# Performance work log

Hardware: AMD Instinct MI355X
Metric: run time of the kernel (lower is better)

The kernel has to match this reference:

```python
import jax, jax.numpy as jnp
import numpy as np
import math

B, N, E, H, DEPTH, MLP_RATIO, A = 8, 1024, 768, 12, 6, 4, 7
F = MLP_RATIO * E


def _get_attention_slopes(n):
    def p2(n):
        start = 2 ** (-2 ** (-(math.log2(n) - 3)))
        return [start * start ** i for i in range(n)]
    if math.log2(n).is_integer():
        return p2(n)
    c = 2 ** math.floor(math.log2(n))
    return p2(c) + _get_attention_slopes(2 * c)[0::2][: n - c]


def _ln(x, scale, bias, eps=1e-6):
    m = jnp.mean(x, axis=-1, keepdims=True)
    v = jnp.var(x, axis=-1, keepdims=True)
    return (x - m) * jax.lax.rsqrt(v + eps) * scale + bias


def setup_inputs() -> dict:
    key = jax.random.key(0)
    ks = jax.random.split(key, 8)
    s = 0.02
    return {
        "x": jax.random.normal(ks[0], (B, N, E), jnp.float32),
        "ln1_scale": jnp.ones((DEPTH, E), jnp.float32),
        "ln1_bias": jnp.zeros((DEPTH, E), jnp.float32),
        "wqkv": jax.random.normal(ks[1], (DEPTH, E, 3 * E), jnp.float32) * s,
        "bqkv": jnp.zeros((DEPTH, 3 * E), jnp.float32),
        "wo": jax.random.normal(ks[2], (DEPTH, E, E), jnp.float32) * s,
        "bo": jnp.zeros((DEPTH, E), jnp.float32),
        "ln2_scale": jnp.ones((DEPTH, E), jnp.float32),
        "ln2_bias": jnp.zeros((DEPTH, E), jnp.float32),
        "w1": jax.random.normal(ks[3], (DEPTH, E, F), jnp.float32) * s,
        "w2": jax.random.normal(ks[4], (DEPTH, F, E), jnp.float32) * s,
        "lnf_scale": jnp.ones((E,), jnp.float32),
        "lnf_bias": jnp.zeros((E,), jnp.float32),
        "head_w1": jax.random.normal(ks[5], (E, E), jnp.float32) * s,
        "head_b1": jnp.zeros((E,), jnp.float32),
        "head_w2": jax.random.normal(ks[6], (E, A), jnp.float32) * s,
    }


def reference(x, ln1_scale, ln1_bias, wqkv, bqkv, wo, bo, ln2_scale, ln2_bias, w1, w2, lnf_scale, lnf_bias, head_w1, head_b1, head_w2):
    b, n, e = x.shape
    h = H
    dh = e // h
    scale = dh ** (-0.5)
    # ALiBi bias: slopes[h] * key-position (exactly as original code computes it)
    slopes = jnp.asarray(_get_attention_slopes(h), x.dtype)
    pos_bias = slopes[None, :, None, None] * jnp.arange(n, dtype=x.dtype)[None, None, None, :]
    causal = jnp.tril(jnp.ones((n, n), bool))[None, None]  # [1,1,n,n]
    big_neg = jnp.finfo(x.dtype).min

    depth = ln1_scale.shape[0]
    for i in range(depth):
        y = _ln(x, ln1_scale[i], ln1_bias[i])
        qkv = y @ wqkv[i] + bqkv[i]
        q, k, v = jnp.split(qkv, 3, axis=-1)
        q = q.reshape(b, n, h, dh).transpose(0, 2, 1, 3)  # b h n d
        k = k.reshape(b, n, h, dh).transpose(0, 2, 1, 3)
        v = v.reshape(b, n, h, dh).transpose(0, 2, 1, 3)
        att = jnp.einsum('bhnd,bhmd->bhnm', q, k) * scale + pos_bias
        att = jnp.where(causal, att, big_neg)
        att = jax.nn.softmax(att, axis=-1)
        o = jnp.einsum('bhnm,bhmd->bhnd', att, v)
        o = o.transpose(0, 2, 1, 3).reshape(b, n, e)
        x = x + (o @ wo[i] + bo[i])
        y = _ln(x, ln2_scale[i], ln2_bias[i])
        y = jax.nn.gelu(y @ w1[i])  # flax default: tanh-approx gelu; FF has no bias
        x = x + y @ w2[i]
    x = _ln(x, lnf_scale, lnf_bias)
    actions = jax.nn.relu(x @ head_w1 + head_b1) @ head_w2
    return actions
```

## Files before the change

### kernel.cpp

```cpp
#include <hip/hip_runtime.h>
#include <hip/hip_bf16.h>
#include <cstdint>

#define DEV __device__ __forceinline__

typedef __bf16 bf16x8 __attribute__((ext_vector_type(8)));
typedef float f32x4 __attribute__((ext_vector_type(4)));
typedef unsigned short u16;
typedef u16 u16x8 __attribute__((ext_vector_type(8)));
typedef u16 u16x4 __attribute__((ext_vector_type(4)));
typedef uint32_t u32x2 __attribute__((ext_vector_type(2)));
typedef uint32_t u32x4 __attribute__((ext_vector_type(4)));

DEV u16 f2bf(float f) {
  union { float f; uint32_t u; } a; a.f = f;
  uint32_t u = a.u + 0x7fffu + ((a.u >> 16) & 1u);
  return (u16)(u >> 16);
}
DEV float b2f(u16 v) {
  union { uint32_t u; float f; } a; a.u = ((uint32_t)v) << 16;
  return a.f;
}

DEV float fexp2(float x) {
#if __has_builtin(__builtin_amdgcn_exp2f)
  return __builtin_amdgcn_exp2f(x);
#else
  return __expf(x * 0.69314718056f);
#endif
}

DEV uint32_t cvtpk(float lo, float hi) {
  uint32_t r;
  asm("v_cvt_pk_bf16_f32 %0, %1, %2" : "=v"(r) : "v"(lo), "v"(hi));
  return r;
}

DEV void gload16(const void* g, void* lds) {
  __builtin_amdgcn_global_load_lds((__attribute__((address_space(1))) void*)g,
                                   (__attribute__((address_space(3))) void*)lds,
                                   16, 0, 0);
}

struct TMat { const float* src; u16* dst; int K; int N; int t0; };
struct TArgs { TMat m[26]; int nmat; };

__global__ __launch_bounds__(256) void transpose_all(TArgs args) {
  __shared__ float tile[128][65];
  const int bid = blockIdx.x;
  int i = 0;
  #pragma unroll 1
  for (int t = 1; t < args.nmat; ++t) if (bid >= args.m[t].t0) i = t;
  const TMat mm = args.m[i];
  const int tid = threadIdx.x;
  const int tix = bid - mm.t0;
  const int ntx = mm.N >> 6;
  const int n0 = (tix % ntx) << 6, k0 = (tix / ntx) << 7;
  const int lr = tid >> 4, lc4 = (tid & 15) << 2;
  #pragma unroll
  for (int p = 0; p < 8; ++p) {
    const int r = lr + (p << 4);
    f32x4 v = __builtin_nontemporal_load(
        (const f32x4*)(mm.src + (size_t)(k0 + r) * mm.N + n0 + lc4));
    *(f32x4*)&tile[r][lc4] = v;
  }
  __syncthreads();
  const int ks8 = (tid & 15) << 3;
  #pragma unroll
  for (int p = 0; p < 4; ++p) {
    const int n = (tid >> 4) + (p << 4);
    float v[8];
    #pragma unroll
    for (int u = 0; u < 8; ++u) v[u] = tile[ks8 + u][n];
    u32x4 o;
    o[0] = cvtpk(v[0], v[1]); o[1] = cvtpk(v[2], v[3]);
    o[2] = cvtpk(v[4], v[5]); o[3] = cvtpk(v[6], v[7]);
    __builtin_nontemporal_store(
        o, (u32x4*)(mm.dst + (size_t)(n0 + n) * mm.K + k0 + ks8));
  }
}

__global__ __launch_bounds__(256) void f2b_kernel(const f32x4* __restrict__ in,
                                                  u32x4* __restrict__ out, int n8) {
  const int i = blockIdx.x * 256 + threadIdx.x;
  if (i >= n8) return;
  f32x4 a = __builtin_nontemporal_load(in + 2 * i);
  f32x4 b = __builtin_nontemporal_load(in + 2 * i + 1);
  u32x4 o;
  o[0] = cvtpk(a[0], a[1]); o[1] = cvtpk(a[2], a[3]);
  o[2] = cvtpk(b[0], b[1]); o[3] = cvtpk(b[2], b[3]);
  __builtin_nontemporal_store(o, out + i);
}

__global__ __launch_bounds__(256) void ln_kernel(const u16* __restrict__ x,
                                                 const float* __restrict__ sc,
                                                 const float* __restrict__ bi,
                                                 u16* __restrict__ y, int Mtok) {
  const int bid = blockIdx.x;
  const int tok = ((bid & 7) << 10) + ((bid >> 3) << 2) + (threadIdx.x >> 6);
  const int l = threadIdx.x & 63;
  if (tok >= Mtok) return;
  const u16* row = x + (size_t)tok * 768;
  u16x8 v0 = *(const u16x8*)(row + l * 8);
  u16x4 v1 = *(const u16x4*)(row + 512 + l * 4);
  float f[12];
  #pragma unroll
  for (int i = 0; i < 8; ++i) f[i] = b2f(v0[i]);
  #pragma unroll
  for (int i = 0; i < 4; ++i) f[8 + i] = b2f(v1[i]);
  float s = 0.f, q = 0.f;
  #pragma unroll
  for (int i = 0; i < 12; ++i) { s += f[i]; q += f[i] * f[i]; }
  #pragma unroll
  for (int off = 1; off < 64; off <<= 1) { s += __shfl_xor(s, off); q += __shfl_xor(q, off); }
  const float mean = s * (1.f / 768.f);
  const float var = q * (1.f / 768.f) - mean * mean;
  const float r = rsqrtf(var + 1e-6f);
  float4 s0 = *(const float4*)(sc + l * 8);
  float4 s1 = *(const float4*)(sc + l * 8 + 4);
  float4 s2 = *(const float4*)(sc + 512 + l * 4);
  float4 b0 = *(const float4*)(bi + l * 8);
  float4 b1 = *(const float4*)(bi + l * 8 + 4);
  float4 b2 = *(const float4*)(bi + 512 + l * 4);
  float g[12];
  g[0] = (f[0]-mean)*r*s0.x + b0.x;  g[1] = (f[1]-mean)*r*s0.y + b0.y;
  g[2] = (f[2]-mean)*r*s0.z + b0.z;  g[3] = (f[3]-mean)*r*s0.w + b0.w;
  g[4] = (f[4]-mean)*r*s1.x + b1.x;  g[5] = (f[5]-mean)*r*s1.y + b1.y;
  g[6] = (f[6]-mean)*r*s1.z + b1.z;  g[7] = (f[7]-mean)*r*s1.w + b1.w;
  g[8] = (f[8]-mean)*r*s2.x + b2.x;  g[9] = (f[9]-mean)*r*s2.y + b2.y;
  g[10] = (f[10]-mean)*r*s2.z + b2.z; g[11] = (f[11]-mean)*r*s2.w + b2.w;
  u16* yr = y + (size_t)tok * 768;
  u32x4 o;
  o[0] = cvtpk(g[0], g[1]); o[1] = cvtpk(g[2], g[3]);
  o[2] = cvtpk(g[4], g[5]); o[3] = cvtpk(g[6], g[7]);
  *(u32x4*)(yr + l * 8) = o;
  u32x2 o2; o2[0] = cvtpk(g[8], g[9]); o2[1] = cvtpk(g[10], g[11]);
  *(u32x2*)(yr + 512 + l * 4) = o2;
}

enum { EPI_BF16 = 0, EPI_RESID = 1, EPI_GELU = 2, EPI_RELU = 3 };

__global__ __launch_bounds__(1024, 2) void gemm128(
    const u16* __restrict__ A, const u16* __restrict__ Bt,
    const float* __restrict__ bias, const u16* __restrict__ residB,
    u16* __restrict__ outB, int N, int K, int nxb, int epi) {
  __shared__ u16 smem[32768];
  const int tid = threadIdx.x;
  const int w = tid >> 6, l = tid & 63;

  const int nwg = gridDim.x;
  const int flat = blockIdx.x;
  const int wg = (flat & 7) * (nwg >> 3) + (flat >> 3);
  const int bx = wg % nxb, by = wg / nxb;
  const int m0 = by << 7, n0 = bx << 7;

  const int wr = (w >> 2) << 5;
  const int wc = (w & 3) << 5;
  const int cl = l & 15, g = l >> 4;
  f32x4 acc[2][2] = {};

  const int lrow = l >> 3;
  const int scol = ((l & 7) ^ lrow) << 3;
  const u16* agp = A  + (size_t)(m0 + (w << 3) + lrow) * K + scol;
  const u16* bgp = Bt + (size_t)(n0 + (w << 3) + lrow) * K + scol;
  const int ldso = w << 9;
  const int nkt = K >> 6;

  gload16(agp, &smem[ldso]);
  gload16(bgp, &smem[16384 + ldso]);

  const int sw = cl & 7;
  for (int kt = 0; kt < nkt; ++kt) {
    const int cur = kt & 1;
    if (kt + 1 < nkt) {
      const size_t koff = (size_t)(kt + 1) << 6;
      const int nb = (cur ^ 1) << 13;
      gload16(agp + koff, &smem[nb + ldso]);
      gload16(bgp + koff, &smem[16384 + nb + ldso]);
      asm volatile("s_waitcnt vmcnt(2)" ::: "memory");
    } else {
      asm volatile("s_waitcnt vmcnt(0)" ::: "memory");
    }
    __builtin_amdgcn_s_barrier();
    __builtin_amdgcn_sched_barrier(0);
    const u16* Ab = &smem[cur << 13];
    const u16* Bb = &smem[16384 + (cur << 13)];
    #pragma unroll
    for (int ks = 0; ks < 2; ++ks) {
      bf16x8 af[2], bfr[2];
      const int ps = (((ks << 2) | g) ^ sw) << 3;
      #pragma unroll
      for (int mt = 0; mt < 2; ++mt)
        af[mt] = *(const bf16x8*)(Ab + ((wr + mt * 16 + cl) << 6) + ps);
      #pragma unroll
      for (int nt = 0; nt < 2; ++nt)
        bfr[nt] = *(const bf16x8*)(Bb + ((wc + nt * 16 + cl) << 6) + ps);
      #pragma unroll
      for (int mt = 0; mt < 2; ++mt)
        #pragma unroll
        for (int nt = 0; nt < 2; ++nt)
          acc[mt][nt] = __builtin_amdgcn_mfma_f32_16x16x32_bf16(af[mt], bfr[nt], acc[mt][nt], 0, 0, 0);
    }
    asm volatile("s_waitcnt lgkmcnt(0)" ::: "memory");
    __builtin_amdgcn_s_barrier();
  }

  float* scr = (float*)smem + w * 544;
  const int rg = g << 2;
  const int er = l >> 2;
  const int ec0 = (l & 3) << 3;
  #pragma unroll
  for (int mt = 0; mt < 2; ++mt) {
    #pragma unroll
    for (int nt = 0; nt < 2; ++nt)
      #pragma unroll
      for (int j = 0; j < 4; ++j)
        scr[(rg + j) * 34 + nt * 16 + cl] = acc[mt][nt][j];
    const int grow = m0 + wr + mt * 16 + er;
    const int gcol = n0 + wc + ec0;
    float v[8];
    #pragma unroll
    for (int u = 0; u < 8; ++u) v[u] = scr[er * 34 + ec0 + u];
    if (bias) {
      #pragma unroll
      for (int u = 0; u < 8; ++u) v[u] += bias[gcol + u];
    }
    if (epi == EPI_RESID) {
      u16x8 rv = *(const u16x8*)(residB + (size_t)grow * N + gcol);
      #pragma unroll
      for (int u = 0; u < 8; ++u) v[u] += b2f(rv[u]);
    } else if (epi == EPI_GELU) {
      #pragma unroll
      for (int u = 0; u < 8; ++u) {
        const float x = v[u];
        const float e = __expf(-(1.5957691216f * x + 0.0713548163f * x * x * x));
        v[u] = x / (1.f + e);
      }
    } else if (epi == EPI_RELU) {
      #pragma unroll
      for (int u = 0; u < 8; ++u) v[u] = fmaxf(v[u], 0.f);
    }
    u32x4 ov;
    ov[0] = cvtpk(v[0], v[1]); ov[1] = cvtpk(v[2], v[3]);
    ov[2] = cvtpk(v[4], v[5]); ov[3] = cvtpk(v[6], v[7]);
    u32x4* op = (u32x4*)(outB + (size_t)grow * N + gcol);
    if (epi == EPI_BF16 || epi == EPI_GELU)
      __builtin_nontemporal_store(ov, op);
    else
      *op = ov;
  }
}

__global__ __launch_bounds__(512, 6) void attn_kernel(const u16* __restrict__ qkv,
                                                      u16* __restrict__ o) {
  __shared__ u16 Ksm[2][4096];
  __shared__ u16 Vt[2][64][68];
  __shared__ u16 P[8][16][72];
  const int flat = blockIdx.x;
  const int b = flat & 7;
  const int rr = flat >> 3;
  const int h = rr >> 3;
  const int j = rr & 7;
  const int tid = threadIdx.x;
  const int w = tid >> 6, l = tid & 63;
  const int cl = l & 15, lg = l >> 4;
  const int qtile = (w < 4) ? j : 15 - j;
  const int q0 = qtile * 64 + (w & 3) * 16;
  const int rowg = q0 + cl;
  const float log2e = 1.44269504f;
  const float scale2 = 0.125f * log2e;
  const float slope = (h < 8) ? exp2f(-(float)(h + 1)) : exp2f(-0.5f - (float)(h - 8));
  const float slope2 = slope * log2e;
  const size_t rs_ = 2304;
  const size_t bbase = (size_t)b * 1024 * rs_;

  const u16* qp = qkv + bbase + (size_t)rowg * rs_ + h * 64 + lg * 8;
  bf16x8 qa0 = *(const bf16x8*)qp;
  bf16x8 qa1 = *(const bf16x8*)(qp + 32);

  float m_r = -1e30f, l_r = 0.f;
  f32x4 oacc[4];
  #pragma unroll
  for (int d = 0; d < 4; ++d) oacc[d] = (f32x4){0.f, 0.f, 0.f, 0.f};

  const u16* ksrc = qkv + bbase + (size_t)(tid >> 3) * rs_ + 768 + h * 64 +
                    (((tid & 7) ^ ((tid >> 3) & 7)) << 3);
  const int vd0 = w << 3;
  const u16* vbase = qkv + bbase + (size_t)l * rs_ + 1536 + h * 64 + vd0;

  const int nkv = 16 - j;
  gload16(ksrc, &Ksm[0][w << 9]);
  u16x8 vreg = *(const u16x8*)vbase;
  __syncthreads();

  const int sw = cl & 7;
  const int ps0 = (lg ^ sw) << 3;
  const int ps1 = ps0 ^ 32;

  for (int kv = 0; kv < nkv; ++kv) {
    const int buf = kv & 1;
    #pragma unroll
    for (int i = 0; i < 8; ++i) Vt[buf][vd0 + i][l] = vreg[i];
    u16x8 vnext = vreg;
    if (kv + 1 < nkv) {
      gload16(ksrc + (size_t)(kv + 1) * 64 * rs_, &Ksm[buf ^ 1][w << 9]);
      vnext = *(const u16x8*)(vbase + (size_t)(kv + 1) * 64 * rs_);
    }

    const bool active = (kv <= qtile);
    bf16x8 pa0, pa1;
    if (active) {
      const u16* Kb = &Ksm[buf][0];
      f32x4 pp[4];
      float pm = -3.0e38f;
      __builtin_amdgcn_s_setprio(1);
      #pragma unroll
      for (int nt = 0; nt < 4; ++nt) {
        const int row = nt * 16 + cl;
        bf16x8 bk0 = *(const bf16x8*)(Kb + (row << 6) + ps0);
        bf16x8 bk1 = *(const bf16x8*)(Kb + (row << 6) + ps1);
        f32x4 s = (f32x4){0.f, 0.f, 0.f, 0.f};
        s = __builtin_amdgcn_mfma_f32_16x16x32_bf16(bk0, qa0, s, 0, 0, 0);
        s = __builtin_amdgcn_mfma_f32_16x16x32_bf16(bk1, qa1, s, 0, 0, 0);
        const int kb = kv * 64 + nt * 16 + (lg << 2);
        #pragma unroll
        for (int jj = 0; jj < 4; ++jj) {
          const int colg = kb + jj;
          float v = s[jj] * scale2 + slope2 * (float)colg;
          pp[nt][jj] = (colg <= rowg) ? v : -3.0e38f;
        }
        pm = fmaxf(pm, fmaxf(fmaxf(pp[nt][0], pp[nt][1]),
                             fmaxf(pp[nt][2], pp[nt][3])));
      }
      __builtin_amdgcn_s_setprio(0);
      pm = fmaxf(pm, __shfl_xor(pm, 16));
      pm = fmaxf(pm, __shfl_xor(pm, 32));
      if (!__all(pm <= m_r + 11.54f)) {
        const float mnew = fmaxf(m_r, pm);
        const float al = fexp2(m_r - mnew);
        m_r = mnew;
        l_r *= al;
        float a4[4];
        #pragma unroll
        for (int jj = 0; jj < 4; ++jj) a4[jj] = __shfl(al, (lg << 2) + jj);
        #pragma unroll
        for (int d = 0; d < 4; ++d)
          #pragma unroll
          for (int jj = 0; jj < 4; ++jj) oacc[d][jj] *= a4[jj];
      }
      float rs = 0.f;
      #pragma unroll
      for (int nt = 0; nt < 4; ++nt) {
        #pragma unroll
        for (int jj = 0; jj < 4; ++jj) {
          float p = fexp2(pp[nt][jj] - m_r);
          pp[nt][jj] = p;
          rs += p;
        }
      }
      rs += __shfl_xor(rs, 16);
      rs += __shfl_xor(rs, 32);
      l_r += rs;
      #pragma unroll
      for (int nt = 0; nt < 4; ++nt) {
        u32x2 pr;
        pr[0] = cvtpk(pp[nt][0], pp[nt][1]);
        pr[1] = cvtpk(pp[nt][2], pp[nt][3]);
        *(u32x2*)&P[w][cl][nt * 16 + (lg << 2)] = pr;
      }
      pa0 = *(const bf16x8*)&P[w][cl][lg * 8];
      pa1 = *(const bf16x8*)&P[w][cl][32 + lg * 8];
    }

    __syncthreads();

    if (active) {
      __builtin_amdgcn_s_setprio(1);
      #pragma unroll
      for (int d = 0; d < 4; ++d) {
        bf16x8 bv0 = *(const bf16x8*)&Vt[buf][d * 16 + cl][lg * 8];
        bf16x8 bv1 = *(const bf16x8*)&Vt[buf][d * 16 + cl][32 + lg * 8];
        oacc[d] = __builtin_amdgcn_mfma_f32_16x16x32_bf16(pa0, bv0, oacc[d], 0, 0, 0);
        oacc[d] = __builtin_amdgcn_mfma_f32_16x16x32_bf16(pa1, bv1, oacc[d], 0, 0, 0);
      }
      __builtin_amdgcn_s_setprio(0);
    }
    vreg = vnext;
  }

  const float linv = 1.f / l_r;
  float i4[4];
  #pragma unroll
  for (int jj = 0; jj < 4; ++jj) i4[jj] = __shfl(linv, (lg << 2) + jj);
  u16* op = o + ((size_t)b * 1024 + q0) * 768 + h * 64;
  #pragma unroll
  for (int d = 0; d < 4; ++d)
    #pragma unroll
    for (int jj = 0; jj < 4; ++jj)
      op[(size_t)((lg << 2) + jj) * 768 + d * 16 + cl] = f2bf(oacc[d][jj] * i4[jj]);
}

__global__ __launch_bounds__(256) void head2_kernel(const u16* __restrict__ act,
                                                    const float* __restrict__ w,
                                                    float* __restrict__ out, int Mtok) {
  const int bid = blockIdx.x;
  const int tok = ((bid & 7) << 10) + ((bid >> 3) << 2) + (threadIdx.x >> 6);
  const int l = threadIdx.x & 63;
  if (tok >= Mtok) return;
  float s[7] = {0.f, 0.f, 0.f, 0.f, 0.f, 0.f, 0.f};
  const u16* ar = act + (size_t)tok * 768;
  #pragma unroll
  for (int i = 0; i < 12; ++i) {
    const int k = l + i * 64;
    const float a = b2f(ar[k]);
    #pragma unroll
    for (int j = 0; j < 7; ++j) s[j] += a * w[k * 7 + j];
  }
  #pragma unroll
  for (int off = 32; off; off >>= 1)
    #pragma unroll
    for (int j = 0; j < 7; ++j) s[j] += __shfl_down(s[j], off);
  if (l == 0) {
    #pragma unroll
    for (int j = 0; j < 7; ++j) out[(size_t)tok * 7 + j] = s[j];
  }
}

extern "C" void kernel_launch(void* const* d_in, const int* in_sizes, int n_in,
                              void* d_out, int out_size, void* d_ws, size_t ws_size,
                              hipStream_t stream) {
  const float* x_in = (const float*)d_in[0];
  const float* ln1s = (const float*)d_in[1];
  const float* ln1b = (const float*)d_in[2];
  const float* wqkv = (const float*)d_in[3];
  const float* bqkv = (const float*)d_in[4];
  const float* wo   = (const float*)d_in[5];
  const float* bo   = (const float*)d_in[6];
  const float* ln2s = (const float*)d_in[7];
  const float* ln2b = (const float*)d_in[8];
  const float* w1   = (const float*)d_in[9];
  const float* w2   = (const float*)d_in[10];
  const float* lnfs = (const float*)d_in[11];
  const float* lnfb = (const float*)d_in[12];
  const float* hw1  = (const float*)d_in[13];
  const float* hb1  = (const float*)d_in[14];
  const float* hw2  = (const float*)d_in[15];
  float* out = (float*)d_out;

  const int Mtok = 8192, E = 768, E3 = 2304, F = 3072, DEPTH = 6;

  char* ws = (char*)d_ws;
  size_t off = 0;
  auto alloc = [&](size_t bytes) -> char* {
    char* p = ws + off; off += (bytes + 255) & ~(size_t)255; return p;
  };
  u16*  wqkvt = (u16*)alloc((size_t)DEPTH * E3 * E * 2);
  u16*  wot   = (u16*)alloc((size_t)DEPTH * E * E * 2);
  u16*  w1t   = (u16*)alloc((size_t)DEPTH * F * E * 2);
  u16*  w2t   = (u16*)alloc((size_t)DEPTH * E * F * 2);
  u16*  hw1t  = (u16*)alloc((size_t)E * E * 2);
  u16*  xb    = (u16*)alloc((size_t)Mtok * E * 2);
  u16*  yb    = (u16*)alloc((size_t)Mtok * E * 2);
  u16*  big   = (u16*)alloc((size_t)Mtok * F * 2);
  (void)ws_size; (void)in_sizes; (void)n_in; (void)out_size;

  TArgs ta; int nm = 0; int t0 = 0;
  auto add = [&](const float* s, u16* d, int K, int N) {
    ta.m[nm].src = s; ta.m[nm].dst = d; ta.m[nm].K = K; ta.m[nm].N = N; ta.m[nm].t0 = t0;
    t0 += (N / 64) * (K / 128); ++nm;
  };
  for (int i = 0; i < DEPTH; ++i) add(wqkv + (size_t)i * E * E3, wqkvt + (size_t)i * E3 * E, E, E3);
  for (int i = 0; i < DEPTH; ++i) add(wo + (size_t)i * E * E, wot + (size_t)i * E * E, E, E);
  for (int i = 0; i < DEPTH; ++i) add(w1 + (size_t)i * E * F, w1t + (size_t)i * F * E, E, F);
  for (int i = 0; i < DEPTH; ++i) add(w2 + (size_t)i * F * E, w2t + (size_t)i * E * F, F, E);
  add(hw1, hw1t, E, E);
  ta.nmat = nm;
  transpose_all<<<t0, 256, 0, stream>>>(ta);

  f2b_kernel<<<(Mtok * E / 8 + 255) / 256, 256, 0, stream>>>(
      (const f32x4*)x_in, (u32x4*)xb, Mtok * E / 8);

  u16* qkvb = big;
  for (int i = 0; i < DEPTH; ++i) {
    ln_kernel<<<Mtok / 4, 256, 0, stream>>>(xb, ln1s + i * E, ln1b + i * E, yb, Mtok);
    gemm128<<<18 * 64, 1024, 0, stream>>>(yb, wqkvt + (size_t)i * E3 * E, bqkv + (size_t)i * E3,
                                          nullptr, qkvb, E3, E, 18, EPI_BF16);
    attn_kernel<<<768, 512, 0, stream>>>(qkvb, yb);
    gemm128<<<6 * 64, 1024, 0, stream>>>(yb, wot + (size_t)i * E * E, bo + (size_t)i * E,
                                         xb, xb, E, E, 6, EPI_RESID);
    ln_kernel<<<Mtok / 4, 256, 0, stream>>>(xb, ln2s + i * E, ln2b + i * E, yb, Mtok);
    gemm128<<<24 * 64, 1024, 0, stream>>>(yb, w1t + (size_t)i * F * E, nullptr,
                                          nullptr, big, F, E, 24, EPI_GELU);
    gemm128<<<6 * 64, 1024, 0, stream>>>(big, w2t + (size_t)i * E * F, nullptr,
                                         xb, xb, E, F, 6, EPI_RESID);
  }
  ln_kernel<<<Mtok / 4, 256, 0, stream>>>(xb, lnfs, lnfb, yb, Mtok);
  gemm128<<<6 * 64, 1024, 0, stream>>>(yb, hw1t, hb1, nullptr, big,
                                       E, E, 6, EPI_RELU);
  head2_kernel<<<Mtok / 4, 256, 0, stream>>>(big, hw2, out, Mtok);
}
```

Measured before the change: 1.353 ms.

## Add 256x256-tile GEMM kernel for QKV and MLP-up projections

Introduces a gemm256 kernel with 256x256 output tiles (each wave computes a 64x64 block via 4x4 MFMA fragments), a 32-wide K step with double buffering, and a swizzled LDS scratch for the epilogue. The QKV and FFN-up GEMMs now use it, while gemm128 keeps only the residual/relu paths. Larger tiles raise arithmetic intensity and cut global traffic per FLOP. The cost is more accumulator registers, shorter K-steps with more barriers per FLOP, and fewer workgroups (288 and 384), which may underfill the GPU.

```diff
diff --git a/kernel.cpp b/kernel.cpp
--- a/kernel.cpp
+++ b/kernel.cpp
@@ -140,6 +140,109 @@
 
 enum { EPI_BF16 = 0, EPI_RESID = 1, EPI_GELU = 2, EPI_RELU = 3 };
 
+__global__ __launch_bounds__(1024, 4) void gemm256(
+    const u16* __restrict__ A, const u16* __restrict__ Bt,
+    const float* __restrict__ bias, u16* __restrict__ outB,
+    int N, int K, int nxb, int epi) {
+  __shared__ u16 smem[32768];
+  const int tid = threadIdx.x;
+  const int w = tid >> 6, l = tid & 63;
+
+  const int nwg = gridDim.x;
+  const int flat = blockIdx.x;
+  const int wg = (flat & 7) * (nwg >> 3) + (flat >> 3);
+  const int bx = wg % nxb, by = wg / nxb;
+  const int m0 = by << 8, n0 = bx << 8;
+
+  const int wr = (w >> 2) << 6;
+  const int wc = (w & 3) << 6;
+  const int cl = l & 15, g = l >> 4;
+  f32x4 acc[4][4] = {};
+
+  const int srow = tid >> 2;
+  const int scol = (((tid & 3) ^ ((tid >> 2) & 3) ^ ((tid >> 4) & 3)) << 3);
+  const u16* agp = A  + (size_t)(m0 + srow) * K + scol;
+  const u16* bgp = Bt + (size_t)(n0 + srow) * K + scol;
+  const int ldso = w << 9;
+  const int nkt = K >> 5;
+
+  gload16(agp, &smem[ldso]);
+  gload16(bgp, &smem[16384 + ldso]);
+
+  const int ps = ((g ^ (cl & 3) ^ ((cl >> 2) & 3)) << 3);
+  for (int kt = 0; kt < nkt; ++kt) {
+    const int cur = kt & 1;
+    if (kt + 1 < nkt) {
+      const int koff = (kt + 1) << 5;
+      const int nb = (cur ^ 1) << 13;
+      gload16(agp + koff, &smem[nb + ldso]);
+      gload16(bgp + koff, &smem[16384 + nb + ldso]);
+      asm volatile("s_waitcnt vmcnt(2)" ::: "memory");
+    } else {
+      asm volatile("s_waitcnt vmcnt(0)" ::: "memory");
+    }
+    __builtin_amdgcn_s_barrier();
+    __builtin_amdgcn_sched_barrier(0);
+    const u16* Ab = &smem[cur << 13];
+    const u16* Bb = &smem[16384 + (cur << 13)];
+    bf16x8 af[4], bfr[4];
+    #pragma unroll
+    for (int mt = 0; mt < 4; ++mt)
+      af[mt] = *(const bf16x8*)(Ab + ((wr + mt * 16 + cl) << 5) + ps);
+    #pragma unroll
+    for (int nt = 0; nt < 4; ++nt)
+      bfr[nt] = *(const bf16x8*)(Bb + ((wc + nt * 16 + cl) << 5) + ps);
+    #pragma unroll
+    for (int mt = 0; mt < 4; ++mt)
+      #pragma unroll
+      for (int nt = 0; nt < 4; ++nt)
+        acc[mt][nt] = __builtin_amdgcn_mfma_f32_16x16x32_bf16(af[mt], bfr[nt], acc[mt][nt], 0, 0, 0);
+    asm volatile("s_waitcnt lgkmcnt(0)" ::: "memory");
+    __builtin_amdgcn_s_barrier();
+  }
+
+  float* scr = (float*)smem + w * 1024;
+  const int rg = g << 2;
+  const int er = l >> 3;
+  const int ec0 = (l & 7) << 3;
+  #pragma unroll
+  for (int mt = 0; mt < 4; ++mt) {
+    #pragma unroll
+    for (int nt = 0; nt < 4; ++nt)
+      #pragma unroll
+      for (int j = 0; j < 4; ++j) {
+        const int row = rg + j;
+        scr[row * 64 + ((nt * 16 + cl) ^ ((row & 7) << 3))] = acc[mt][nt][j];
+      }
+    #pragma unroll
+    for (int t = 0; t < 2; ++t) {
+      const int r = (t << 3) + er;
+      const int grow = m0 + wr + mt * 16 + r;
+      const int gcol = n0 + wc + ec0;
+      const int pc = (ec0 ^ ((r & 7) << 3));
+      float v[8];
+      #pragma unroll
+      for (int u = 0; u < 8; ++u) v[u] = scr[r * 64 + pc + u];
+      if (bias) {
+        #pragma unroll
+        for (int u = 0; u < 8; ++u) v[u] += bias[gcol + u];
+      }
+      if (epi == EPI_GELU) {
+        #pragma unroll
+        for (int u = 0; u < 8; ++u) {
+          const float x = v[u];
+          const float e = __expf(-(1.5957691216f * x + 0.0713548163f * x * x * x));
+          v[u] = x / (1.f + e);
+        }
+      }
+      u32x4 ov;
+      ov[0] = cvtpk(v[0], v[1]); ov[1] = cvtpk(v[2], v[3]);
+      ov[2] = cvtpk(v[4], v[5]); ov[3] = cvtpk(v[6], v[7]);
+      __builtin_nontemporal_store(ov, (u32x4*)(outB + (size_t)grow * N + gcol));
+    }
+  }
+}
+
 __global__ __launch_bounds__(1024, 2) void gemm128(
     const u16* __restrict__ A, const u16* __restrict__ Bt,
     const float* __restrict__ bias, const u16* __restrict__ residB,
@@ -229,13 +332,6 @@
       u16x8 rv = *(const u16x8*)(residB + (size_t)grow * N + gcol);
       #pragma unroll
       for (int u = 0; u < 8; ++u) v[u] += b2f(rv[u]);
-    } else if (epi == EPI_GELU) {
-      #pragma unroll
-      for (int u = 0; u < 8; ++u) {
-        const float x = v[u];
-        const float e = __expf(-(1.5957691216f * x + 0.0713548163f * x * x * x));
-        v[u] = x / (1.f + e);
-      }
     } else if (epi == EPI_RELU) {
       #pragma unroll
       for (int u = 0; u < 8; ++u) v[u] = fmaxf(v[u], 0.f);
@@ -244,10 +340,7 @@
     ov[0] = cvtpk(v[0], v[1]); ov[1] = cvtpk(v[2], v[3]);
     ov[2] = cvtpk(v[4], v[5]); ov[3] = cvtpk(v[6], v[7]);
     u32x4* op = (u32x4*)(outB + (size_t)grow * N + gcol);
-    if (epi == EPI_BF16 || epi == EPI_GELU)
-      __builtin_nontemporal_store(ov, op);
-    else
-      *op = ov;
+    *op = ov;
   }
 }
 
@@ -483,14 +576,14 @@
   u16* qkvb = big;
   for (int i = 0; i < DEPTH; ++i) {
     ln_kernel<<<Mtok / 4, 256, 0, stream>>>(xb, ln1s + i * E, ln1b + i * E, yb, Mtok);
-    gemm128<<<18 * 64, 1024, 0, stream>>>(yb, wqkvt + (size_t)i * E3 * E, bqkv + (size_t)i * E3,
-                                          nullptr, qkvb, E3, E, 18, EPI_BF16);
+    gemm256<<<9 * 32, 1024, 0, stream>>>(yb, wqkvt + (size_t)i * E3 * E,
+                                         bqkv + (size_t)i * E3, qkvb, E3, E, 9, EPI_BF16);
     attn_kernel<<<768, 512, 0, stream>>>(qkvb, yb);
     gemm128<<<6 * 64, 1024, 0, stream>>>(yb, wot + (size_t)i * E * E, bo + (size_t)i * E,
                                          xb, xb, E, E, 6, EPI_RESID);
     ln_kernel<<<Mtok / 4, 256, 0, stream>>>(xb, ln2s + i * E, ln2b + i * E, yb, Mtok);
-    gemm128<<<24 * 64, 1024, 0, stream>>>(yb, w1t + (size_t)i * F * E, nullptr,
-                                          nullptr, big, F, E, 24, EPI_GELU);
+    gemm256<<<12 * 32, 1024, 0, stream>>>(yb, w1t + (size_t)i * F * E,
+                                          nullptr, big, F, E, 12, EPI_GELU);
     gemm128<<<6 * 64, 1024, 0, stream>>>(big, w2t + (size_t)i * E * F, nullptr,
                                          xb, xb, E, F, 6, EPI_RESID);
   }
```

Result: slower. 1.553 ms (+14.8%).
